# Kernel tuning notes

Measured on AMD Instinct MI355X. Metric: run time of the kernel, lower is better.

Reference implementation:

```python
import jax, jax.numpy as jnp
from jax import lax
import numpy as np
import math

B, H, W = 4, 1080, 1080
MINSIZE = 20
FACTOR = 0.709
THRESH = 0.6
STRIDE = 2.0
CELL = 12.0


def get_scales():
    scales = []
    scale = CELL / MINSIZE
    m = scale * min(H, W)
    while m >= 12:
        scales.append(scale)
        scale *= FACTOR
        m *= FACTOR
    return scales


def setup_inputs() -> dict:
    key = jax.random.key(0)
    ks = jax.random.split(key, 6)
    init = lambda k, shp: jax.random.normal(k, shp, jnp.float32) * 0.1
    return {
        "inputs": jax.random.uniform(ks[0], (B, H, W, 3), jnp.float32) * 255.0,
        "w1": init(ks[1], (3, 3, 3, 10)), "b1": jnp.zeros((10,), jnp.float32),
        "w2": init(ks[2], (3, 3, 10, 16)), "b2": jnp.zeros((16,), jnp.float32),
        "w3": init(ks[3], (3, 3, 16, 32)), "b3": jnp.zeros((32,), jnp.float32),
        "wp": init(ks[4], (1, 1, 32, 2)), "bp": jnp.zeros((2,), jnp.float32),
        "wr": init(ks[5], (1, 1, 32, 4)), "br": jnp.zeros((4,), jnp.float32),
    }


def _conv(x, w, pad):
    return lax.conv_general_dilated(x, w, (1, 1), pad,
                                    dimension_numbers=('NHWC', 'HWIO', 'NHWC'))


def _lrelu(x):
    return jnp.where(x > 0, x, 0.3 * x)  # keras LeakyReLU default alpha=0.3


def _pnet(x, w1, b1, w2, b2, w3, b3, wp, bp, wr, br):
    x = _lrelu(_conv(x, w1, 'VALID') + b1)
    x = lax.reduce_window(x, -jnp.inf, lax.max, (1, 2, 2, 1), (1, 2, 2, 1), 'SAME')
    x = _lrelu(_conv(x, w2, 'VALID') + b2)
    x = _lrelu(_conv(x, w3, 'VALID') + b3)
    probs = jax.nn.softmax(_conv(x, wp, 'SAME') + bp, axis=-1)
    reg = _conv(x, wr, 'SAME') + br
    return probs, reg


def reference(inputs, w1, b1, w2, b2, w3, b3, wp, bp, wr, br):
    boxes_all, reg_all, mask_all = [], [], []
    b = inputs.shape[0]
    for scale in get_scales():
        hs, ws = int(math.ceil(H * scale)), int(math.ceil(W * scale))
        img = (jax.image.resize(inputs, (b, hs, ws, 3), 'bilinear') - 127.5) / 128.0
        probs, reg = _pnet(img, w1, b1, w2, b2, w3, b3, wp, bp, wr, br)
        score = probs[..., 1]  # [B, h, w]
        _, h, w = score.shape
        rr, cc = jnp.meshgrid(jnp.arange(h, dtype=jnp.float32),
                              jnp.arange(w, dtype=jnp.float32), indexing='ij')
        pos = jnp.stack([rr, cc], axis=-1)  # grid positions (row, col)
        ul = jnp.round((pos * STRIDE + 1.0) / scale)          # upper-left corner
        dr = jnp.round((pos * STRIDE + CELL - 1.0 + 1.0) / scale)  # down-right corner
        boxes = jnp.concatenate([
            jnp.broadcast_to(ul, (b, h, w, 2)),
            jnp.broadcast_to(dr, (b, h, w, 2)),
            score[..., None]], axis=-1)  # [B, h, w, 5]
        boxes_all.append(boxes.reshape(b, h * w, 5))
        reg_all.append(reg.reshape(b, h * w, 4))
        mask_all.append((score >= THRESH).reshape(b, h * w))  # rows getBBox would gather
    return (jnp.concatenate(boxes_all, axis=1),
            jnp.concatenate(reg_all, axis=1),
            jnp.concatenate(mask_all, axis=1))
```

## Files before the change

kernel.cpp:

```cpp
#include <hip/hip_runtime.h>
#include <math.h>

#define TPB 256
#define C3T 16

struct SP {
    int  n;
    int  blkBase[13];
    int  xBase[13];
    int  hs[12];
    int  ph[12];
    int  istr[12];
    int  wstr[12];
    float inv[12];
    float rinv[12];
    float scl[12];
    long wOff[12];
    long jOff[12];
    long tmpOff[12];
    long imgOff[12];
    long pOff[12];
    long qOff[12];
    long base[12];
};

__device__ __forceinline__ float lrelu(float x) { return x > 0.f ? x : 0.3f * x; }

__device__ __forceinline__ int find_scale(const SP& p, int bb) {
    int s = 0;
#pragma unroll
    for (int k = 1; k < 12; k++)
        if (k < p.n && bb >= p.blkBase[k]) s = k;
    return s;
}

__global__ __launch_bounds__(TPB) void k_wt(float* __restrict__ wsb, SP p) {
    int s = blockIdx.x;
    int hs = p.hs[s];
    int wstr = p.wstr[s];
    float inv = p.inv[s], rinv = p.rinv[s];
    float* wt = wsb + p.wOff[s];
    int* jt = (int*)wsb + p.jOff[s];
    for (int x = threadIdx.x; x < hs; x += TPB) {
        float c = ((float)x + 0.5f) * inv - 0.5f;
        int jlo = (int)floorf(c - inv);
        if (jlo < 0) jlo = 0;
        if (jlo > 1080 - wstr) jlo = 1080 - wstr;
        float sum = 0.f;
        for (int k = 0; k < wstr; k++) {
            float w = fmaxf(0.f, 1.f - fabsf(c - (float)(jlo + k)) * rinv);
            sum += w;
        }
        float rt = 1.f / sum;
        for (int k = 0; k < wstr; k++) {
            float w = fmaxf(0.f, 1.f - fabsf(c - (float)(jlo + k)) * rinv);
            wt[k * hs + x] = w * rt;
        }
        jt[x] = jlo;
    }
}

__global__ __launch_bounds__(TPB) void k_hres1(const float* __restrict__ in,
                                               float* __restrict__ wsb, SP p) {
    __shared__ float row[3240];
    __shared__ float sInv[12], sRinv[12];
    __shared__ int sWstr[12], sXB[13];
    __shared__ long sOff[12];
    int r = blockIdx.x;
    if (threadIdx.x < 12) {
        int s = threadIdx.x;
        if (s < p.n) {
            sInv[s] = p.inv[s];
            sRinv[s] = p.rinv[s];
            sWstr[s] = p.wstr[s];
            sXB[s] = p.xBase[s];
            sOff[s] = p.tmpOff[s] + (long)r * p.istr[s];
        }
    }
    if (threadIdx.x == 0) sXB[p.n] = p.xBase[p.n];
    const float4* src = (const float4*)(in + (long)r * 3240);
    float4* row4 = (float4*)row;
    for (int ch = threadIdx.x; ch < 810; ch += TPB) row4[ch] = src[ch];
    __syncthreads();
    int xTot = p.xBase[p.n];
    for (int ft = threadIdx.x; ft < xTot; ft += TPB) {
        int s = 0;
#pragma unroll
        for (int k = 1; k < 12; k++)
            if (k < p.n && ft >= sXB[k]) s = k;
        int x = ft - sXB[s];
        float inv = sInv[s], rinv = sRinv[s];
        int wstr = sWstr[s];
        float c = ((float)x + 0.5f) * inv - 0.5f;
        int jlo = (int)floorf(c - inv);
        if (jlo < 0) jlo = 0;
        int jmax = 1080 - wstr;
        if (jlo > jmax) jlo = jmax;
        float d = c - (float)jlo;
        const float* pr = row + jlo * 3;
        float n0 = 0.f, n1 = 0.f, n2 = 0.f, tw = 0.f;
        for (int k = 0; k < wstr; k++) {
            float w = fmaxf(0.f, fmaf(-fabsf(d), rinv, 1.f));
            tw += w;
            n0 += w * pr[0]; n1 += w * pr[1]; n2 += w * pr[2];
            d -= 1.f; pr += 3;
        }
        float rt = 1.f / tw;
        float* o = wsb + sOff[s] + x * 3;
        o[0] = n0 * rt;
        o[1] = n1 * rt;
        o[2] = n2 * rt;
    }
}

__global__ __launch_bounds__(TPB) void k_vres2(float* __restrict__ wsb, SP p) {
    __shared__ float wsm[152];
    int bb = blockIdx.x;
    int s = find_scale(p, bb);
    int hs = p.hs[s];
    int istr = p.istr[s];
    int wstr = p.wstr[s];
    int r = bb - p.blkBase[s];
    int i = r % hs;
    int b = r / hs;
    int jlo = ((const int*)wsb + p.jOff[s])[i];
    const float* wt = wsb + p.wOff[s];
    for (int k = threadIdx.x; k < wstr; k += TPB)
        wsm[k] = wt[k * hs + i];
    __syncthreads();
    int W4 = istr >> 2;
    const float4* src0 = (const float4*)(wsb + p.tmpOff[s] + ((long)b * 1080 + jlo) * istr);
    float4* dst = (float4*)(wsb + p.imgOff[s] + (long)r * istr);
    for (int ch = threadIdx.x; ch < W4; ch += TPB) {
        float4 acc = {0.f, 0.f, 0.f, 0.f};
        const float4* sp = src0 + ch;
        for (int k = 0; k < wstr; k++) {
            float w = wsm[k];
            float4 v = sp[(long)k * W4];
            acc.x += w * v.x; acc.y += w * v.y; acc.z += w * v.z; acc.w += w * v.w;
        }
        float4 o;
        o.x = (acc.x - 127.5f) * 0.0078125f;
        o.y = (acc.y - 127.5f) * 0.0078125f;
        o.z = (acc.z - 127.5f) * 0.0078125f;
        o.w = (acc.w - 127.5f) * 0.0078125f;
        dst[ch] = o;
    }
}

__global__ __launch_bounds__(TPB) void k_c1p(float* __restrict__ wsb,
                                             const float* __restrict__ w1,
                                             const float* __restrict__ b1, SP p) {
    int bb = blockIdx.x;
    int s = find_scale(p, bb);
    int hs = p.hs[s];
    int istr = p.istr[s];
    int ph = p.ph[s];
    int t = (bb - p.blkBase[s]) * TPB + threadIdx.x;
    if (t >= 4 * ph * ph) return;
    int px = t % ph;
    int rem = t / ph;
    int pi = rem % ph;
    int b = rem / ph;
    const float* img = wsb + p.imgOff[s] + (long)b * hs * istr;
    int r0 = 2 * pi, c0 = 2 * px;
    float im[4][4][3];
#pragma unroll
    for (int dy = 0; dy < 4; dy++) {
        int r = r0 + dy;
#pragma unroll
        for (int dx = 0; dx < 4; dx++) {
            int cc = c0 + dx;
            if (r < hs && cc < hs) {
                const float* pp = img + (long)r * istr + cc * 3;
                im[dy][dx][0] = pp[0]; im[dy][dx][1] = pp[1]; im[dy][dx][2] = pp[2];
            } else {
                im[dy][dx][0] = 0.f; im[dy][dx][1] = 0.f; im[dy][dx][2] = 0.f;
            }
        }
    }
    int ch = hs - 2;
    bool v01 = (c0 + 1) < ch;
    bool v10 = (r0 + 1) < ch;
    bool v11 = v01 && v10;
    float* P = wsb + p.pOff[s] + (((long)b * ph + pi) * ph + px) * 10;
#pragma unroll 1
    for (int oc = 0; oc < 10; ++oc) {
        float bias = b1[oc];
        float a00 = bias, a01 = bias, a10 = bias, a11 = bias;
#pragma unroll
        for (int ky = 0; ky < 3; ky++)
#pragma unroll
            for (int kx = 0; kx < 3; kx++)
#pragma unroll
                for (int ic = 0; ic < 3; ic++) {
                    float w = w1[((ky * 3 + kx) * 3 + ic) * 10 + oc];
                    a00 += im[ky][kx][ic] * w;
                    a01 += im[ky][kx + 1][ic] * w;
                    a10 += im[ky + 1][kx][ic] * w;
                    a11 += im[ky + 1][kx + 1][ic] * w;
                }
        float mx = lrelu(a00);
        if (v01) mx = fmaxf(mx, lrelu(a01));
        if (v10) mx = fmaxf(mx, lrelu(a10));
        if (v11) mx = fmaxf(mx, lrelu(a11));
        P[oc] = mx;
    }
}

__global__ __launch_bounds__(TPB) void k_c2(float* __restrict__ wsb,
                                            const float* __restrict__ w2,
                                            const float* __restrict__ b2, SP p) {
    int bb = blockIdx.x;
    int s = find_scale(p, bb);
    int ph = p.ph[s];
    int qh = ph - 2;
    int t = (bb - p.blkBase[s]) * TPB + threadIdx.x;
    if (t >= 4 * qh * qh) return;
    int qx = t % qh;
    int rem = t / qh;
    int qi = rem % qh;
    int b = rem / qh;
    const float* P = wsb + p.pOff[s] + (long)b * ph * ph * 10;
    float acc[16];
#pragma unroll
    for (int oc = 0; oc < 16; oc++) acc[oc] = b2[oc];
#pragma unroll 1
    for (int pos = 0; pos < 9; pos++) {
        int ky = pos / 3, kx = pos - ky * 3;
        const float* pp = P + ((long)(qi + ky) * ph + (qx + kx)) * 10;
        float v[10];
#pragma unroll
        for (int h = 0; h < 5; h++) {
            float2 v2 = *(const float2*)(pp + 2 * h);
            v[2 * h] = v2.x; v[2 * h + 1] = v2.y;
        }
#pragma unroll
        for (int ic = 0; ic < 10; ic++)
#pragma unroll
            for (int oc = 0; oc < 16; oc++)
                acc[oc] += v[ic] * w2[(pos * 10 + ic) * 16 + oc];
    }
    float* Q = wsb + p.qOff[s] + (((long)b * qh + qi) * qh + qx) * 16;
    float4* Q4 = (float4*)Q;
#pragma unroll
    for (int h = 0; h < 4; h++) {
        float4 o;
        o.x = lrelu(acc[4 * h + 0]); o.y = lrelu(acc[4 * h + 1]);
        o.z = lrelu(acc[4 * h + 2]); o.w = lrelu(acc[4 * h + 3]);
        Q4[h] = o;
    }
}

__global__ __launch_bounds__(TPB) void k_c3h(float* __restrict__ wsb,
                                             const float* __restrict__ w3,
                                             const float* __restrict__ b3,
                                             const float* __restrict__ wp,
                                             const float* __restrict__ bpb,
                                             const float* __restrict__ wr,
                                             const float* __restrict__ brb,
                                             float* __restrict__ out, long N, SP p) {
    __shared__ float Qs[18 * 18 * 20];
    int bb = blockIdx.x;
    int s = find_scale(p, bb);
    int ph = p.ph[s];
    int qh = ph - 2;
    int oh = ph - 4;
    int ntx = (oh + C3T - 1) / C3T;
    int tile = bb - p.blkBase[s];
    int tx = tile % ntx;
    int rem = tile / ntx;
    int ty = rem % ntx;
    int b = rem / ntx;
    int x0 = tx * C3T, y0 = ty * C3T;
    const float* Q = wsb + p.qOff[s] + (long)b * qh * qh * 16;
    for (int site = threadIdx.x; site < 324; site += TPB) {
        int lr = site / 18, lc = site - lr * 18;
        int gr = y0 + lr; if (gr > qh - 1) gr = qh - 1;
        int gc = x0 + lc; if (gc > qh - 1) gc = qh - 1;
        const float4* srcp = (const float4*)(Q + ((long)gr * qh + gc) * 16);
        float4* dstp = (float4*)&Qs[(lr * 18 + lc) * 20];
#pragma unroll
        for (int h = 0; h < 4; h++) dstp[h] = srcp[h];
    }
    __syncthreads();
    int ox = threadIdx.x & 15, oy = threadIdx.x >> 4;
    int x = x0 + ox, y = y0 + oy;
    float acc[32];
#pragma unroll
    for (int oc = 0; oc < 32; oc++) acc[oc] = b3[oc];
#pragma unroll 1
    for (int pos = 0; pos < 9; pos++) {
        int ky = pos / 3, kx = pos - ky * 3;
        const float4* cp = (const float4*)&Qs[((oy + ky) * 18 + ox + kx) * 20];
        float v[16];
#pragma unroll
        for (int h = 0; h < 4; h++) {
            float4 v4 = cp[h];
            v[4 * h] = v4.x; v[4 * h + 1] = v4.y; v[4 * h + 2] = v4.z; v[4 * h + 3] = v4.w;
        }
#pragma unroll
        for (int ic = 0; ic < 16; ic++)
#pragma unroll
            for (int oc = 0; oc < 32; oc++)
                acc[oc] += v[ic] * w3[(pos * 16 + ic) * 32 + oc];
    }
    if (x >= oh || y >= oh) return;
    float p0 = bpb[0], p1 = bpb[1];
    float r0 = brb[0], r1 = brb[1], r2 = brb[2], r3 = brb[3];
#pragma unroll
    for (int ic = 0; ic < 32; ic++) {
        float v = lrelu(acc[ic]);
        p0 += v * wp[ic * 2 + 0]; p1 += v * wp[ic * 2 + 1];
        r0 += v * wr[ic * 4 + 0]; r1 += v * wr[ic * 4 + 1];
        r2 += v * wr[ic * 4 + 2]; r3 += v * wr[ic * 4 + 3];
    }
    float mx = fmaxf(p0, p1);
    float e0 = expf(p0 - mx), e1 = expf(p1 - mx);
    float score = e1 / (e0 + e1);
    float sclf = p.scl[s];
    long idx = p.base[s] + (long)y * oh + x;
    long g = (long)b * N + idx;
    float fy = (float)y, fx = (float)x;
    float* ob = out + g * 5;
    ob[0] = rintf((2.f * fy + 1.f) / sclf);
    ob[1] = rintf((2.f * fx + 1.f) / sclf);
    ob[2] = rintf((2.f * fy + 12.f) / sclf);
    ob[3] = rintf((2.f * fx + 12.f) / sclf);
    ob[4] = score;
    float* orr = out + N * 20 + g * 4;
    orr[0] = r0; orr[1] = r1; orr[2] = r2; orr[3] = r3;
    out[N * 36 + g] = (score >= 0.6f) ? 1.f : 0.f;
}

static int fill_blocks(SP& q, const int* cnt) {
    int acc = 0;
    for (int s = 0; s < q.n; s++) {
        q.blkBase[s] = acc;
        acc += (cnt[s] + TPB - 1) / TPB;
    }
    q.blkBase[q.n] = acc;
    return acc;
}

static int fill_rows(SP& q, const int* cnt) {
    int acc = 0;
    for (int s = 0; s < q.n; s++) {
        q.blkBase[s] = acc;
        acc += cnt[s];
    }
    q.blkBase[q.n] = acc;
    return acc;
}

extern "C" void kernel_launch(void* const* d_in, const int* in_sizes, int n_in,
                              void* d_out, int out_size, void* d_ws, size_t ws_size,
                              hipStream_t stream) {
    const float* in = (const float*)d_in[0];
    const float* w1 = (const float*)d_in[1];
    const float* b1 = (const float*)d_in[2];
    const float* w2 = (const float*)d_in[3];
    const float* b2 = (const float*)d_in[4];
    const float* w3 = (const float*)d_in[5];
    const float* b3 = (const float*)d_in[6];
    const float* wp = (const float*)d_in[7];
    const float* bp = (const float*)d_in[8];
    const float* wr = (const float*)d_in[9];
    const float* br = (const float*)d_in[10];
    float* ws = (float*)d_ws;
    float* out = (float*)d_out;

    double sc = 12.0 / 20.0, m = sc * 1080.0;
    int ns = 0;
    double scl[12];
    while (m >= 12.0 && ns < 12) { scl[ns++] = sc; sc *= 0.709; m *= 0.709; }

    int hs[12], ph[12], istr[12], wstr[12];
    long base[12];
    long N = 0;
    for (int s = 0; s < ns; s++) {
        hs[s] = (int)ceil(1080.0 * scl[s]);
        ph[s] = (hs[s] - 1) / 2;
        istr[s] = ((hs[s] * 3 + 3) / 4) * 4;
        double invd = 1080.0 / (double)hs[s];
        wstr[s] = (int)ceil(2.0 * invd) + 2;
        if (wstr[s] > 1080) wstr[s] = 1080;
    }
    for (int s = 0; s < ns; s++) {
        int oh = ph[s] - 4;
        base[s] = N;
        N += (long)oh * oh;
    }

    long wOff[12], jOff[12], tmpOff[12], imgOff[12], pOff[12], qOff[12];
    long off = 0;
    for (int s = 0; s < ns; s++) { wOff[s] = off; off += (long)wstr[s] * hs[s]; }
    for (int s = 0; s < ns; s++) { jOff[s] = off; off += hs[s]; }
    off = (off + 3) & ~3L;
    long tabEnd = off;
    for (int s = 0; s < ns; s++) { tmpOff[s] = off; off += 4L * 1080 * istr[s]; }
    for (int s = 0; s < ns; s++) { imgOff[s] = off; off += 4L * hs[s] * istr[s]; }
    for (int s = 0; s < ns; s++) { pOff[s] = off; off += 4L * ph[s] * ph[s] * 10; }
    for (int s = 0; s < ns; s++) { qOff[s] = off; off += 4L * (ph[s] - 2) * (ph[s] - 2) * 16; }
    bool batched = (ws_size >= (size_t)off * 4);
    if (!batched) {
        long TMP2MAX = 4L * 1080 * istr[0];
        long IMGMAX = 4L * hs[0] * istr[0];
        long PMAX = 4L * ph[0] * ph[0] * 10;
        for (int s = 0; s < ns; s++) {
            tmpOff[s] = tabEnd;
            imgOff[s] = tabEnd + TMP2MAX;
            pOff[s] = tabEnd + TMP2MAX + IMGMAX;
            qOff[s] = tabEnd + TMP2MAX + IMGMAX + PMAX;
        }
    }

    SP pAll;
    pAll.n = ns;
    for (int s = 0; s < ns; s++) {
        pAll.hs[s] = hs[s]; pAll.ph[s] = ph[s]; pAll.istr[s] = istr[s];
        pAll.wstr[s] = wstr[s];
        pAll.inv[s] = (float)(1080.0 / (double)hs[s]);
        pAll.rinv[s] = (float)((double)hs[s] / 1080.0);
        pAll.scl[s] = (float)scl[s];
        pAll.wOff[s] = wOff[s]; pAll.jOff[s] = jOff[s];
        pAll.tmpOff[s] = tmpOff[s]; pAll.imgOff[s] = imgOff[s];
        pAll.pOff[s] = pOff[s]; pAll.qOff[s] = qOff[s];
        pAll.base[s] = base[s];
    }
    k_wt<<<ns, TPB, 0, stream>>>(ws, pAll);

    int gcount = batched ? 1 : ns;
    for (int g = 0; g < gcount; ++g) {
        int s0 = batched ? 0 : g;
        int cnt = batched ? ns : 1;
        SP p;
        p.n = cnt;
        int xacc = 0;
        for (int k = 0; k < cnt; k++) {
            int s = s0 + k;
            p.hs[k] = hs[s]; p.ph[k] = ph[s]; p.istr[k] = istr[s];
            p.wstr[k] = wstr[s];
            p.xBase[k] = xacc; xacc += hs[s];
            p.inv[k] = (float)(1080.0 / (double)hs[s]);
            p.rinv[k] = (float)((double)hs[s] / 1080.0);
            p.scl[k] = (float)scl[s];
            p.wOff[k] = wOff[s]; p.jOff[k] = jOff[s];
            p.tmpOff[k] = tmpOff[s]; p.imgOff[k] = imgOff[s];
            p.pOff[k] = pOff[s]; p.qOff[k] = qOff[s];
            p.base[k] = base[s];
        }
        p.xBase[cnt] = xacc;
        int crow[12], c3[12], c4[12], c5[12];
        for (int k = 0; k < cnt; k++) {
            int s = s0 + k;
            int PH = ph[s], QH = PH - 2, OH = PH - 4;
            int NTX = (OH + C3T - 1) / C3T;
            crow[k] = 4 * hs[s];
            c3[k] = 4 * PH * PH;
            c4[k] = 4 * QH * QH;
            c5[k] = 4 * NTX * NTX;
        }
        int nb;
        SP ps = p;
        k_hres1<<<4 * 1080, TPB, 0, stream>>>(in, ws, p);
        ps = p; nb = fill_rows(ps, crow);
        k_vres2<<<nb, TPB, 0, stream>>>(ws, ps);
        ps = p; nb = fill_blocks(ps, c3);
        k_c1p<<<nb, TPB, 0, stream>>>(ws, w1, b1, ps);
        ps = p; nb = fill_blocks(ps, c4);
        k_c2<<<nb, TPB, 0, stream>>>(ws, w2, b2, ps);
        ps = p; nb = fill_rows(ps, c5);
        k_c3h<<<nb, TPB, 0, stream>>>(ws, w3, b3, wp, bp, wr, br, out, N, ps);
    }
}
```

Baseline: 431.9 us.

## Add banded vertical resize with shared-memory ring buffer for large scales

Adds a new vertical-resize kernel for scales with small filter windows. Each block processes a band of output rows and a strip of columns, keeping the input rows in a shared-memory ring buffer so overlapping source rows are loaded once rather than once per output row. It uses a newly written transposed weight table and splits the scales between the new kernel and the old per-row kernel. The horizontal resize also pads pixels to float4 in shared memory, trading one vectorized load for three scalar loads. The new path adds extra weight-table writes and more syncthreads per row.

```diff
diff --git a/kernel.cpp b/kernel.cpp
--- a/kernel.cpp
+++ b/kernel.cpp
@@ -3,6 +3,8 @@
 
 #define TPB 256
 #define C3T 16
+#define RBAND 48
+#define RWMAX 16
 
 struct SP {
     int  n;
@@ -16,6 +18,7 @@
     float rinv[12];
     float scl[12];
     long wOff[12];
+    long wtTOff[12];
     long jOff[12];
     long tmpOff[12];
     long imgOff[12];
@@ -24,6 +27,14 @@
     long base[12];
 };
 
+struct SPR {
+    int n;
+    int blkBase[7];
+    int hs[6], istr[6], wstr[6], nst[6], nbd[6];
+    float inv[6];
+    long tmpOff[6], imgOff[6], wtTOff[6];
+};
+
 __device__ __forceinline__ float lrelu(float x) { return x > 0.f ? x : 0.3f * x; }
 
 __device__ __forceinline__ int find_scale(const SP& p, int bb) {
@@ -40,6 +51,7 @@
     int wstr = p.wstr[s];
     float inv = p.inv[s], rinv = p.rinv[s];
     float* wt = wsb + p.wOff[s];
+    float* wtT = wsb + p.wtTOff[s];
     int* jt = (int*)wsb + p.jOff[s];
     for (int x = threadIdx.x; x < hs; x += TPB) {
         float c = ((float)x + 0.5f) * inv - 0.5f;
@@ -53,8 +65,9 @@
         }
         float rt = 1.f / sum;
         for (int k = 0; k < wstr; k++) {
-            float w = fmaxf(0.f, 1.f - fabsf(c - (float)(jlo + k)) * rinv);
-            wt[k * hs + x] = w * rt;
+            float w = fmaxf(0.f, 1.f - fabsf(c - (float)(jlo + k)) * rinv) * rt;
+            wt[k * hs + x] = w;
+            wtT[x * wstr + k] = w;
         }
         jt[x] = jlo;
     }
@@ -62,7 +75,7 @@
 
 __global__ __launch_bounds__(TPB) void k_hres1(const float* __restrict__ in,
                                                float* __restrict__ wsb, SP p) {
-    __shared__ float row[3240];
+    __shared__ float4 row4[1080];
     __shared__ float sInv[12], sRinv[12];
     __shared__ int sWstr[12], sXB[13];
     __shared__ long sOff[12];
@@ -78,9 +91,12 @@
         }
     }
     if (threadIdx.x == 0) sXB[p.n] = p.xBase[p.n];
-    const float4* src = (const float4*)(in + (long)r * 3240);
-    float4* row4 = (float4*)row;
-    for (int ch = threadIdx.x; ch < 810; ch += TPB) row4[ch] = src[ch];
+    const float* src = in + (long)r * 3240;
+    for (int px = threadIdx.x; px < 1080; px += TPB) {
+        const float* q = src + px * 3;
+        float4 v; v.x = q[0]; v.y = q[1]; v.z = q[2]; v.w = 0.f;
+        row4[px] = v;
+    }
     __syncthreads();
     int xTot = p.xBase[p.n];
     for (int ft = threadIdx.x; ft < xTot; ft += TPB) {
@@ -97,19 +113,79 @@
         int jmax = 1080 - wstr;
         if (jlo > jmax) jlo = jmax;
         float d = c - (float)jlo;
-        const float* pr = row + jlo * 3;
         float n0 = 0.f, n1 = 0.f, n2 = 0.f, tw = 0.f;
         for (int k = 0; k < wstr; k++) {
             float w = fmaxf(0.f, fmaf(-fabsf(d), rinv, 1.f));
             tw += w;
-            n0 += w * pr[0]; n1 += w * pr[1]; n2 += w * pr[2];
-            d -= 1.f; pr += 3;
+            float4 v = row4[jlo + k];
+            n0 += w * v.x; n1 += w * v.y; n2 += w * v.z;
+            d -= 1.f;
         }
         float rt = 1.f / tw;
         float* o = wsb + sOff[s] + x * 3;
         o[0] = n0 * rt;
         o[1] = n1 * rt;
         o[2] = n2 * rt;
+    }
+}
+
+__global__ __launch_bounds__(TPB) void k_vres2r(float* __restrict__ wsb, SPR p) {
+    __shared__ float4 ring[RWMAX * TPB];
+    int bb = blockIdx.x;
+    int s = 0;
+#pragma unroll
+    for (int k = 1; k < 6; k++)
+        if (k < p.n && bb >= p.blkBase[k]) s = k;
+    int tile = bb - p.blkBase[s];
+    int hs = p.hs[s], istr = p.istr[s], wstr = p.wstr[s];
+    int nst = p.nst[s], nbd = p.nbd[s];
+    float inv = p.inv[s];
+    int st = tile % nst;
+    int rem = tile / nst;
+    int bd = rem % nbd;
+    int b = rem / nbd;
+    int col = st * TPB + threadIdx.x;
+    int W4 = istr >> 2;
+    bool act = col < W4;
+    const float* tmp2 = wsb + p.tmpOff[s] + (long)b * 1080 * istr;
+    float* img = wsb + p.imgOff[s] + (long)b * hs * istr;
+    const float* wtT = wsb + p.wtTOff[s];
+    int i0 = bd * RBAND;
+    int i1 = i0 + RBAND; if (i1 > hs) i1 = hs;
+    int loaded = -1;
+    for (int i = i0; i < i1; ++i) {
+        float c = ((float)i + 0.5f) * inv - 0.5f;
+        int jl = (int)floorf(c - inv);
+        if (jl < 0) jl = 0;
+        int jm = 1080 - wstr;
+        if (jl > jm) jl = jm;
+        int jh = jl + wstr - 1;
+        int jstart = (i == i0) ? jl : (loaded + 1 > jl ? loaded + 1 : jl);
+        __syncthreads();
+        if (act) {
+            for (int j = jstart; j <= jh; ++j)
+                ring[(j % wstr) * TPB + threadIdx.x] =
+                    *(const float4*)(tmp2 + (long)j * istr + col * 4);
+        }
+        loaded = jh;
+        __syncthreads();
+        if (act) {
+            float a0 = 0.f, a1 = 0.f, a2 = 0.f, a3 = 0.f;
+            int slot = jl % wstr;
+            const float* wrow = wtT + i * wstr;
+            for (int k = 0; k < wstr; k++) {
+                float w = wrow[k];
+                float4 v = ring[slot * TPB + threadIdx.x];
+                a0 += w * v.x; a1 += w * v.y; a2 += w * v.z; a3 += w * v.w;
+                slot++; if (slot == wstr) slot = 0;
+            }
+            float4 o;
+            o.x = (a0 - 127.5f) * 0.0078125f;
+            o.y = (a1 - 127.5f) * 0.0078125f;
+            o.z = (a2 - 127.5f) * 0.0078125f;
+            o.w = (a3 - 127.5f) * 0.0078125f;
+            *(float4*)(img + (long)i * istr + col * 4) = o;
+        }
     }
 }
 
@@ -392,9 +468,10 @@
         N += (long)oh * oh;
     }
 
-    long wOff[12], jOff[12], tmpOff[12], imgOff[12], pOff[12], qOff[12];
+    long wOff[12], wtTOff[12], jOff[12], tmpOff[12], imgOff[12], pOff[12], qOff[12];
     long off = 0;
     for (int s = 0; s < ns; s++) { wOff[s] = off; off += (long)wstr[s] * hs[s]; }
+    for (int s = 0; s < ns; s++) { wtTOff[s] = off; off += (long)wstr[s] * hs[s]; }
     for (int s = 0; s < ns; s++) { jOff[s] = off; off += hs[s]; }
     off = (off + 3) & ~3L;
     long tabEnd = off;
@@ -423,7 +500,7 @@
         pAll.inv[s] = (float)(1080.0 / (double)hs[s]);
         pAll.rinv[s] = (float)((double)hs[s] / 1080.0);
         pAll.scl[s] = (float)scl[s];
-        pAll.wOff[s] = wOff[s]; pAll.jOff[s] = jOff[s];
+        pAll.wOff[s] = wOff[s]; pAll.wtTOff[s] = wtTOff[s]; pAll.jOff[s] = jOff[s];
         pAll.tmpOff[s] = tmpOff[s]; pAll.imgOff[s] = imgOff[s];
         pAll.pOff[s] = pOff[s]; pAll.qOff[s] = qOff[s];
         pAll.base[s] = base[s];
@@ -445,18 +522,58 @@
             p.inv[k] = (float)(1080.0 / (double)hs[s]);
             p.rinv[k] = (float)((double)hs[s] / 1080.0);
             p.scl[k] = (float)scl[s];
-            p.wOff[k] = wOff[s]; p.jOff[k] = jOff[s];
+            p.wOff[k] = wOff[s]; p.wtTOff[k] = wtTOff[s]; p.jOff[k] = jOff[s];
             p.tmpOff[k] = tmpOff[s]; p.imgOff[k] = imgOff[s];
             p.pOff[k] = pOff[s]; p.qOff[k] = qOff[s];
             p.base[k] = base[s];
         }
         p.xBase[cnt] = xacc;
-        int crow[12], c3[12], c4[12], c5[12];
+
+        SPR pr; pr.n = 0;
+        SP pold; pold.n = 0;
+        int oldRows[12];
+        {
+            int racc = 0, oacc = 0;
+            for (int k = 0; k < cnt; k++) {
+                int s = s0 + k;
+                if (wstr[s] <= RWMAX && pr.n < 6) {
+                    int ri = pr.n;
+                    int W4 = istr[s] >> 2;
+                    pr.hs[ri] = hs[s]; pr.istr[ri] = istr[s]; pr.wstr[ri] = wstr[s];
+                    pr.nst[ri] = (W4 + TPB - 1) / TPB;
+                    pr.nbd[ri] = (hs[s] + RBAND - 1) / RBAND;
+                    pr.inv[ri] = (float)(1080.0 / (double)hs[s]);
+                    pr.tmpOff[ri] = tmpOff[s]; pr.imgOff[ri] = imgOff[s];
+                    pr.wtTOff[ri] = wtTOff[s];
+                    pr.blkBase[ri] = racc;
+                    racc += pr.nst[ri] * pr.nbd[ri] * 4;
+                    pr.n = ri + 1;
+                } else {
+                    int oi = pold.n;
+                    pold.hs[oi] = hs[s]; pold.ph[oi] = ph[s]; pold.istr[oi] = istr[s];
+                    pold.wstr[oi] = wstr[s];
+                    pold.inv[oi] = (float)(1080.0 / (double)hs[s]);
+                    pold.rinv[oi] = (float)((double)hs[s] / 1080.0);
+                    pold.scl[oi] = (float)scl[s];
+                    pold.wOff[oi] = wOff[s]; pold.wtTOff[oi] = wtTOff[s]; pold.jOff[oi] = jOff[s];
+                    pold.tmpOff[oi] = tmpOff[s]; pold.imgOff[oi] = imgOff[s];
+                    pold.pOff[oi] = pOff[s]; pold.qOff[oi] = qOff[s];
+                    pold.base[oi] = base[s];
+                    oldRows[oi] = 4 * hs[s];
+                    pold.blkBase[oi] = oacc;
+                    oacc += oldRows[oi];
+                    pold.n = oi + 1;
+                }
+            }
+            pr.blkBase[pr.n] = racc;
+            pold.blkBase[pold.n] = oacc;
+        }
+
+        int c3[12], c4[12], c5[12];
         for (int k = 0; k < cnt; k++) {
             int s = s0 + k;
             int PH = ph[s], QH = PH - 2, OH = PH - 4;
             int NTX = (OH + C3T - 1) / C3T;
-            crow[k] = 4 * hs[s];
             c3[k] = 4 * PH * PH;
             c4[k] = 4 * QH * QH;
             c5[k] = 4 * NTX * NTX;
@@ -464,8 +581,10 @@
         int nb;
         SP ps = p;
         k_hres1<<<4 * 1080, TPB, 0, stream>>>(in, ws, p);
-        ps = p; nb = fill_rows(ps, crow);
-        k_vres2<<<nb, TPB, 0, stream>>>(ws, ps);
+        if (pr.n > 0)
+            k_vres2r<<<pr.blkBase[pr.n], TPB, 0, stream>>>(ws, pr);
+        if (pold.n > 0)
+            k_vres2<<<pold.blkBase[pold.n], TPB, 0, stream>>>(ws, pold);
         ps = p; nb = fill_blocks(ps, c3);
         k_c1p<<<nb, TPB, 0, stream>>>(ws, w1, b1, ps);
         ps = p; nb = fill_blocks(ps, c4);
```

After: 506.0 us. +17.2%, slower.
